# Optimization experiments

Hardware: AMD Instinct MI355X
Metric: run time of the kernel (lower is better)

Reference implementation:

```python
import jax, jax.numpy as jnp
import numpy as np

P_OUT = 2048   # num_output_points
K_NN = 32      # num_neighbors
LEAK = 0.2     # LeakyReLU slope in WeightNet


def setup_inputs() -> dict:
    key = jax.random.key(0)
    k1, k2, k3, k4 = jax.random.split(key, 4)
    B, N, D, Cin, Cout, Cmid = 8, 8192, 3, 128, 256, 16
    return {
        "coordinates": jax.random.uniform(k1, (B, N, D), jnp.float32),
        "features": jax.random.normal(k2, (B, N, Cin), jnp.float32),
        "wn_w": jax.random.normal(k3, (Cmid, D), jnp.float32) * 0.1,
        "wn_b": jnp.zeros((Cmid,), jnp.float32),
        "lin_w": jax.random.normal(k4, (Cout, Cin * Cmid), jnp.float32) * 0.02,
        "lin_b": jnp.zeros((Cout,), jnp.float32),
    }


def _fps(coords, num_out):
    """Deterministic farthest point sampling (initial point = index 0)."""
    B, N, _ = coords.shape

    def step(carry, _):
        dist, far = carry
        centroid = jnp.take_along_axis(coords, far[:, None, None], axis=1)  # (B,1,D)
        d = jnp.linalg.norm(coords - centroid, axis=-1)                     # (B,N)
        dist = jnp.minimum(dist, d)
        return (dist, jnp.argmax(dist, axis=-1)), far

    init = (jnp.full((B, N), 1e10, coords.dtype), jnp.zeros((B,), jnp.int32))
    _, idx = jax.lax.scan(step, init, None, length=num_out)
    return jnp.transpose(idx)  # (B, num_out)


def _knn(k, coords, centers):
    # squared L2 via gram trick; monotone in L2 so top-k indices match torch.cdist+topk
    d2 = (jnp.sum(centers ** 2, -1)[:, :, None]
          + jnp.sum(coords ** 2, -1)[:, None, :]
          - 2.0 * jnp.einsum('bpd,bnd->bpn', centers, coords))
    _, idx = jax.lax.top_k(-d2, k)
    return idx  # (B,P,K)


_gather = jax.vmap(lambda pts, idx: pts[idx])  # index_points equivalent


def reference(coordinates, features, wn_w, wn_b, lin_w, lin_b):
    B = coordinates.shape[0]
    samp_idx = _fps(coordinates, P_OUT)                      # (B,P)
    out_coords = _gather(coordinates, samp_idx)              # (B,P,D)
    nbr_idx = _knn(K_NN, coordinates, out_coords)            # (B,P,K)
    group_coords = _gather(coordinates, nbr_idx)             # (B,P,K,D)
    centered = group_coords - out_coords[:, :, None, :]      # (B,P,K,D)
    group_feat = _gather(features, nbr_idx)                  # (B,P,K,Cin)
    # WeightNet: 1x1-conv MLP (single layer) + LeakyReLU(0.2)
    w = jax.nn.leaky_relu(jnp.einsum('bpkd,md->bpkm', centered, wn_w) + wn_b, LEAK)
    # PointConv aggregation: (B,P,Cin,K) @ (B,P,K,Cmid) -> (B,P,Cin,Cmid) -> flatten
    nf = jnp.einsum('bpkc,bpkm->bpcm', group_feat, w).reshape(B, P_OUT, -1)
    nf = nf @ lin_w.T + lin_b                                # (B,P,Cout)
    return out_coords, nf
```

## Files before the change

### kernel.cpp

```cpp
#include <hip/hip_runtime.h>
#include <hip/hip_bf16.h>

#define NB    8
#define NPTS  8192
#define P_OUT 2048
#define KNN   32
#define CIN   128
#define CMID  16
#define COUT  256

typedef __bf16 bf16x8 __attribute__((ext_vector_type(8)));
typedef float  f32x4  __attribute__((ext_vector_type(4)));
typedef float  f32x2  __attribute__((ext_vector_type(2)));

__device__ __forceinline__ float sqrt_rn_f32(float x) { return (float)sqrt((double)x); }

__device__ __forceinline__ unsigned short f2bf(float x) {
    unsigned u = __float_as_uint(x);
    return (unsigned short)((u + 0x7FFFu + ((u >> 16) & 1u)) >> 16);
}

__device__ __forceinline__ float wave_max_dpp(float x) {
    int v, t;
    v = __float_as_int(x);
    t = __builtin_amdgcn_update_dpp(v, v, 0xB1, 0xF, 0xF, false);
    x = fmaxf(x, __int_as_float(t));
    v = __float_as_int(x);
    t = __builtin_amdgcn_update_dpp(v, v, 0x4E, 0xF, 0xF, false);
    x = fmaxf(x, __int_as_float(t));
    v = __float_as_int(x);
    t = __builtin_amdgcn_update_dpp(v, v, 0x141, 0xF, 0xF, false);
    x = fmaxf(x, __int_as_float(t));
    v = __float_as_int(x);
    t = __builtin_amdgcn_update_dpp(v, v, 0x140, 0xF, 0xF, false);
    x = fmaxf(x, __int_as_float(t));
    v = __float_as_int(x);
    t = __builtin_amdgcn_update_dpp(v, v, 0x142, 0xA, 0xF, false);
    x = fmaxf(x, __int_as_float(t));
    v = __float_as_int(x);
    t = __builtin_amdgcn_update_dpp(v, v, 0x143, 0xC, 0xF, false);
    x = fmaxf(x, __int_as_float(t));
    return x;
}

__global__ __launch_bounds__(256) void prep_kernel(const float* __restrict__ coords,
                                                   const float* __restrict__ lin_w,
                                                   float2* __restrict__ zp,
                                                   unsigned short* __restrict__ lwbf) {
    const int i = blockIdx.x * 256 + threadIdx.x;
    if (i < NB * NPTS) {
        const float* pc = coords + (size_t)i * 3;
        const float x = pc[0], y = pc[1], z = pc[2];
        float t = __fmul_rn(x, x);
        t = __fadd_rn(t, __fmul_rn(y, y));
        t = __fadd_rn(t, __fmul_rn(z, z));
        zp[i] = make_float2(z, t);
    }
    if (i < COUT * CIN * CMID) lwbf[i] = f2bf(lin_w[i]);
}

__global__ __launch_bounds__(512) void fps_kernel(const float* __restrict__ coords,
                                                  float* __restrict__ out_coords) {
    #pragma clang fp contract(off)
    const int b    = blockIdx.x;
    const int tid  = threadIdx.x;
    const int lane = tid & 63;
    const int wv   = tid >> 6;
    const float* cb = coords + (size_t)b * (NPTS * 3);
    float* outc = out_coords + (size_t)b * (P_OUT * 3);

    __shared__ __align__(16) float warr[8];
    __shared__ unsigned winslot;
    __shared__ float csl[3];

    f32x2 pxv[8], pyv[8], pzv[8], d2v[8];
    {
        float buf[48];
        const float4* g4 = (const float4*)cb;
        #pragma unroll
        for (int i = 0; i < 12; ++i) {
            float4 v = g4[tid * 12 + i];
            buf[i*4+0] = v.x; buf[i*4+1] = v.y; buf[i*4+2] = v.z; buf[i*4+3] = v.w;
        }
        #pragma unroll
        for (int i = 0; i < 8; ++i) {
            pxv[i] = f32x2{buf[(2*i)*3+0], buf[(2*i+1)*3+0]};
            pyv[i] = f32x2{buf[(2*i)*3+1], buf[(2*i+1)*3+1]};
            pzv[i] = f32x2{buf[(2*i)*3+2], buf[(2*i+1)*3+2]};
            d2v[i] = f32x2{__builtin_inff(), __builtin_inff()};
        }
    }
    if (tid == 0) {
        csl[0] = pxv[0][0]; csl[1] = pyv[0][0]; csl[2] = pzv[0][0];
        winslot = 0xFFFFFFFFu;
    }
    __syncthreads();
    float cx = csl[0], cy = csl[1], cz = csl[2];
    const unsigned base = (unsigned)tid * 16;

    for (int s = 0; s < P_OUT; ++s) {
        if (tid == 0) { outc[s*3+0] = cx; outc[s*3+1] = cy; outc[s*3+2] = cz; }
        if (s == P_OUT - 1) break;

        const f32x2 cx2 = {cx, cx}, cy2 = {cy, cy}, cz2 = {cz, cz};
        f32x2 tmax2 = {0.0f, 0.0f};
        #pragma unroll
        for (int i = 0; i < 8; ++i) {
            const f32x2 dx = pxv[i] - cx2;
            const f32x2 dy = pyv[i] - cy2;
            const f32x2 dz = pzv[i] - cz2;
            f32x2 t = dx * dx;
            t = t + dy * dy;
            t = t + dz * dz;
            const f32x2 nd = __builtin_elementwise_min(d2v[i], t);
            d2v[i] = nd;
            tmax2 = __builtin_elementwise_max(tmax2, nd);
        }
        const float tmax = fmaxf(tmax2[0], tmax2[1]);

        const float wmaxl = wave_max_dpp(tmax);
        if (lane == 63) warr[wv] = wmaxl;
        __syncthreads();

        const float4 q0 = *(const float4*)(warr + 0);
        const float4 q1 = *(const float4*)(warr + 4);
        const float gmax = fmaxf(fmaxf(fmaxf(q0.x, q0.y), fmaxf(q0.z, q0.w)),
                                 fmaxf(fmaxf(q1.x, q1.y), fmaxf(q1.z, q1.w)));
        const float wmax = (wv < 4) ? ((wv < 2) ? (wv ? q0.y : q0.x) : (wv == 2 ? q0.z : q0.w))
                                    : ((wv < 6) ? (wv == 4 ? q1.x : q1.y) : (wv == 6 ? q1.z : q1.w));

        if (__float_as_uint(wmax) + 3u >= __float_as_uint(gmax)) {
            const float s_ = sqrt_rn_f32(gmax);
            float t_lo = gmax;
            const unsigned gb = __float_as_uint(gmax);
            #pragma unroll
            for (int j = 1; j <= 3; ++j) {
                float v = __uint_as_float(gb - j);
                if (sqrt_rn_f32(v) == s_) t_lo = v;
            }
            unsigned cand = 0xFFFFFFFFu;
            #pragma unroll
            for (int i = 7; i >= 0; --i) {
                if (d2v[i][1] >= t_lo) cand = base + 2*i + 1;
                if (d2v[i][0] >= t_lo) cand = base + 2*i;
            }
            if (cand != 0xFFFFFFFFu) atomicMin(&winslot, cand);
        }
        __syncthreads();

        const unsigned widx = winslot;
        if ((widx >> 4) == (unsigned)tid) {
            #pragma unroll
            for (int i = 0; i < 8; ++i) {
                if (widx == base + 2*i)     { csl[0]=pxv[i][0]; csl[1]=pyv[i][0]; csl[2]=pzv[i][0]; }
                if (widx == base + 2*i + 1) { csl[0]=pxv[i][1]; csl[1]=pyv[i][1]; csl[2]=pzv[i][1]; }
            }
        }
        __syncthreads();
        if (tid == 0) winslot = 0xFFFFFFFFu;
        cx = csl[0]; cy = csl[1]; cz = csl[2];
    }
}

__global__ __launch_bounds__(1024) void knn_kernel(const float* __restrict__ coords,
                                                   const float2* __restrict__ zp,
                                                   const float* __restrict__ out_coords,
                                                   int* __restrict__ nbr) {
    const int b     = blockIdx.x & 7;
    const int chunk = blockIdx.x >> 3;
    const int tid   = threadIdx.x;
    const int wv    = tid >> 6, lane = tid & 63;
    __shared__ float2 sxy[NPTS];
    {
        float buf[24];
        const float4* g4 = (const float4*)(coords + (size_t)b * (NPTS * 3));
        #pragma unroll
        for (int i = 0; i < 6; ++i) {
            float4 v = g4[tid * 6 + i];
            buf[i*4+0]=v.x; buf[i*4+1]=v.y; buf[i*4+2]=v.z; buf[i*4+3]=v.w;
        }
        #pragma unroll
        for (int i = 0; i < 8; ++i)
            sxy[tid*8 + i] = make_float2(buf[i*3+0], buf[i*3+1]);
    }
    __syncthreads();
    const float2* zpb = zp + (size_t)b * NPTS;

    for (int ci = 0; ci < 4; ++ci) {
        const int p = chunk * 64 + wv * 4 + ci;
        const float* oc = out_coords + ((size_t)b * P_OUT + p) * 3;
        const float cx = oc[0], cy = oc[1], cz = oc[2];
        const float cc = __fadd_rn(__fadd_rn(__fmul_rn(cx,cx), __fmul_rn(cy,cy)), __fmul_rn(cz,cz));
        float ld2 = __builtin_inff();
        unsigned lidx = 0x7FFFFFFFu;
        for (int j0 = 0; j0 < NPTS; j0 += 64) {
            const int p2 = j0 + lane;
            const float2 xy = sxy[p2];
            const float2 zq = zpb[p2];
            const float dot = fmaf(cz, zq.x, fmaf(cy, xy.y, __fmul_rn(cx, xy.x)));
            const float d2  = __fsub_rn(__fadd_rn(cc, zq.y), __fmul_rn(2.0f, dot));
            const float    T  = __shfl(ld2, 31, 64);
            const unsigned Ti = __shfl(lidx, 31, 64);
            const bool qf = (d2 < T) || (d2 == T && (unsigned)p2 < Ti);
            unsigned long long mask = __ballot(qf);
            while (mask) {
                const int l = __ffsll(mask) - 1;
                const float    cd2  = __shfl(d2, l, 64);
                const unsigned cidx = (unsigned)(j0 + l);
                float    pv = __shfl_up(ld2, 1, 64);
                unsigned pi = __shfl_up(lidx, 1, 64);
                if (lane == 0) { pv = cd2; pi = cidx; }
                const bool mlt = (ld2 < cd2) || (ld2 == cd2 && lidx < cidx);
                const bool plt = (pv  < cd2) || (pv  == cd2 && pi   < cidx);
                ld2  = mlt ? ld2  : (plt ? cd2  : pv);
                lidx = mlt ? lidx : (plt ? cidx : pi);
                mask &= (mask - 1);
            }
        }
        if (lane < KNN) nbr[((size_t)b * P_OUT + p) * KNN + lane] = (int)lidx;
    }
}

__global__ __launch_bounds__(128) void pconv_kernel(const float* __restrict__ coords,
                                                    const float* __restrict__ feats,
                                                    const float* __restrict__ out_coords,
                                                    const int* __restrict__ nbr,
                                                    const float* __restrict__ wn_w,
                                                    const float* __restrict__ wn_b,
                                                    unsigned short* __restrict__ nf) {
    const int bp  = (blockIdx.x & 7) * P_OUT + (blockIdx.x >> 3);
    const int b   = bp >> 11;
    const int tid = threadIdx.x;
    __shared__ __align__(16) float wmat[32][16];
    __shared__ int nidx[32];
    __shared__ float ctr[3];
    if (tid < 32) nidx[tid] = nbr[(size_t)bp * KNN + tid];
    if (tid < 3)  ctr[tid]  = out_coords[(size_t)bp * 3 + tid];
    __syncthreads();
    {
        const int k  = tid >> 2;
        const int m0 = (tid & 3) * 4;
        const int n  = nidx[k];
        const float* pc = coords + ((size_t)b * NPTS + n) * 3;
        const float dx = pc[0] - ctr[0];
        const float dy = pc[1] - ctr[1];
        const float dz = pc[2] - ctr[2];
        #pragma unroll
        for (int mm = 0; mm < 4; ++mm) {
            const int m = m0 + mm;
            float a = dx * wn_w[m*3+0] + dy * wn_w[m*3+1] + dz * wn_w[m*3+2] + wn_b[m];
            wmat[k][m] = (a >= 0.0f) ? a : 0.2f * a;
        }
    }
    __syncthreads();
    const int c = tid;
    float acc[16];
    #pragma unroll
    for (int m = 0; m < 16; ++m) acc[m] = 0.0f;
    const float* fb = feats + (size_t)b * NPTS * CIN;
    #pragma unroll 4
    for (int k = 0; k < 32; ++k) {
        const float f = fb[(size_t)nidx[k] * CIN + c];
        const float4* wr = (const float4*)(&wmat[k][0]);
        const float4 w0 = wr[0], w1 = wr[1], w2 = wr[2], w3 = wr[3];
        acc[0]  += f * w0.x;  acc[1]  += f * w0.y;  acc[2]  += f * w0.z;  acc[3]  += f * w0.w;
        acc[4]  += f * w1.x;  acc[5]  += f * w1.y;  acc[6]  += f * w1.z;  acc[7]  += f * w1.w;
        acc[8]  += f * w2.x;  acc[9]  += f * w2.y;  acc[10] += f * w2.z;  acc[11] += f * w2.w;
        acc[12] += f * w3.x;  acc[13] += f * w3.y;  acc[14] += f * w3.z;  acc[15] += f * w3.w;
    }
    unsigned u[8];
    #pragma unroll
    for (int m = 0; m < 8; ++m) {
        const unsigned lo = f2bf(acc[2*m]);
        const unsigned hi = f2bf(acc[2*m+1]);
        u[m] = lo | (hi << 16);
    }
    uint4* dst = (uint4*)(nf + (size_t)bp * 2048 + c * 16);
    dst[0] = make_uint4(u[0], u[1], u[2], u[3]);
    dst[1] = make_uint4(u[4], u[5], u[6], u[7]);
}

__global__ __launch_bounds__(256) void gemm_kernel(const unsigned short* __restrict__ A,
                                                   const unsigned short* __restrict__ Bw,
                                                   const float* __restrict__ bias,
                                                   float* __restrict__ C) {
    __shared__ __align__(16) unsigned short Als[128 * 40];
    __shared__ __align__(16) unsigned short Bls[128 * 40];
    const int tid = threadIdx.x;
    const int m0  = blockIdx.x * 128;
    const int cb  = blockIdx.y;
    const int wv  = tid >> 6, lane = tid & 63;
    const int wr  = wv >> 1,  wc   = wv & 1;
    const int sr  = tid >> 1;
    const int ko  = (tid & 1) * 16;
    const int rr  = lane & 15, kg = lane >> 4;

    f32x4 acc[4][4] = {};

    for (int kt = 0; kt < 2048 / 32; ++kt) {
        const uint4* as = (const uint4*)(A  + (size_t)(m0 + sr) * 2048 + kt * 32 + ko);
        const uint4 a0 = as[0], a1 = as[1];
        const uint4* bs = (const uint4*)(Bw + (size_t)(cb * 128 + sr) * 2048 + kt * 32 + ko);
        const uint4 b0 = bs[0], b1 = bs[1];
        __syncthreads();
        *(uint4*)(&Als[sr * 40 + ko])     = a0;
        *(uint4*)(&Als[sr * 40 + ko + 8]) = a1;
        *(uint4*)(&Bls[sr * 40 + ko])     = b0;
        *(uint4*)(&Bls[sr * 40 + ko + 8]) = b1;
        __syncthreads();
        bf16x8 af[4], bfv[4];
        #pragma unroll
        for (int i = 0; i < 4; ++i)
            af[i] = *(const bf16x8*)(&Als[(wr*64 + i*16 + rr) * 40 + kg * 8]);
        #pragma unroll
        for (int j = 0; j < 4; ++j)
            bfv[j] = *(const bf16x8*)(&Bls[(wc*64 + j*16 + rr) * 40 + kg * 8]);
        #pragma unroll
        for (int i = 0; i < 4; ++i)
            #pragma unroll
            for (int j = 0; j < 4; ++j)
                acc[i][j] = __builtin_amdgcn_mfma_f32_16x16x32_bf16(af[i], bfv[j], acc[i][j], 0, 0, 0);
    }
    const int rg = lane >> 4;
    #pragma unroll
    for (int j = 0; j < 4; ++j) {
        const int col = cb * 128 + wc * 64 + j * 16 + rr;
        const float bv = bias[col];
        #pragma unroll
        for (int i = 0; i < 4; ++i) {
            const int row = m0 + wr * 64 + i * 16 + rg * 4;
            #pragma unroll
            for (int g = 0; g < 4; ++g)
                C[(size_t)(row + g) * 256 + col] = acc[i][j][g] + bv;
        }
    }
}

extern "C" void kernel_launch(void* const* d_in, const int* in_sizes, int n_in,
                              void* d_out, int out_size, void* d_ws, size_t ws_size,
                              hipStream_t stream) {
    const float* coords = (const float*)d_in[0];
    const float* feats  = (const float*)d_in[1];
    const float* wn_w   = (const float*)d_in[2];
    const float* wn_b   = (const float*)d_in[3];
    const float* lin_w  = (const float*)d_in[4];
    const float* lin_b  = (const float*)d_in[5];

    float* out        = (float*)d_out;
    float* out_coords = out;
    float* out_nf     = out + NB * P_OUT * 3;

    char* ws = (char*)d_ws;
    int*            nbr  = (int*)ws;
    float2*         zp   = (float2*)(ws + ((size_t)2  << 20));
    unsigned short* lwbf = (unsigned short*)(ws + ((size_t)2560 << 10));
    unsigned short* nf   = (unsigned short*)(ws + ((size_t)4  << 20));

    prep_kernel <<<2048, 256, 0, stream>>>(coords, lin_w, zp, lwbf);
    fps_kernel  <<<NB, 512, 0, stream>>>(coords, out_coords);
    knn_kernel  <<<256, 1024, 0, stream>>>(coords, zp, out_coords, nbr);
    pconv_kernel<<<NB * P_OUT, 128, 0, stream>>>(coords, feats, out_coords, nbr, wn_w, wn_b, nf);
    gemm_kernel <<<dim3(128, 2), 256, 0, stream>>>(nf, lwbf, lin_b, out_nf);
}
```

Before: 3.528 ms.

## Cut FPS per-step barriers via double-buffered winner slot and global centroid reload

The FPS loop now double-buffers the atomic winner slot so that resetting it no longer needs its own barrier. The new centroid is read straight from global coordinates by every thread, which replaces the shared-memory broadcast and the third __syncthreads per step. The sqrt-based threshold is computed from the wave-local max before the barrier, hiding that latency. In exchange, each step adds a dependent global (likely L1/L2-hit) load on the serial critical path.

```diff
diff --git a/kernel.cpp b/kernel.cpp
--- a/kernel.cpp
+++ b/kernel.cpp
@@ -70,8 +70,7 @@
     float* outc = out_coords + (size_t)b * (P_OUT * 3);
 
     __shared__ __align__(16) float warr[8];
-    __shared__ unsigned winslot;
-    __shared__ float csl[3];
+    __shared__ unsigned winslot[2];
 
     f32x2 pxv[8], pyv[8], pzv[8], d2v[8];
     {
@@ -90,12 +89,9 @@
             d2v[i] = f32x2{__builtin_inff(), __builtin_inff()};
         }
     }
-    if (tid == 0) {
-        csl[0] = pxv[0][0]; csl[1] = pyv[0][0]; csl[2] = pzv[0][0];
-        winslot = 0xFFFFFFFFu;
-    }
+    if (tid == 0) { winslot[0] = 0xFFFFFFFFu; winslot[1] = 0xFFFFFFFFu; }
+    float cx = cb[0], cy = cb[1], cz = cb[2];
     __syncthreads();
-    float cx = csl[0], cy = csl[1], cz = csl[2];
     const unsigned base = (unsigned)tid * 16;
 
     for (int s = 0; s < P_OUT; ++s) {
@@ -120,23 +116,37 @@
 
         const float wmaxl = wave_max_dpp(tmax);
         if (lane == 63) warr[wv] = wmaxl;
+        const float wmax = __shfl(wmaxl, 63, 64);
+
+        const unsigned wb = __float_as_uint(wmax);
+        const float s_sp = sqrt_rn_f32(wmax);
+        float t_lo_sp = wmax;
+        #pragma unroll
+        for (int j = 1; j <= 3; ++j) {
+            const float v = __uint_as_float(wb - j);
+            if (sqrt_rn_f32(v) == s_sp) t_lo_sp = v;
+        }
         __syncthreads();
+        if (tid == 0) winslot[(s + 1) & 1] = 0xFFFFFFFFu;
 
         const float4 q0 = *(const float4*)(warr + 0);
         const float4 q1 = *(const float4*)(warr + 4);
         const float gmax = fmaxf(fmaxf(fmaxf(q0.x, q0.y), fmaxf(q0.z, q0.w)),
                                  fmaxf(fmaxf(q1.x, q1.y), fmaxf(q1.z, q1.w)));
-        const float wmax = (wv < 4) ? ((wv < 2) ? (wv ? q0.y : q0.x) : (wv == 2 ? q0.z : q0.w))
-                                    : ((wv < 6) ? (wv == 4 ? q1.x : q1.y) : (wv == 6 ? q1.z : q1.w));
-
-        if (__float_as_uint(wmax) + 3u >= __float_as_uint(gmax)) {
-            const float s_ = sqrt_rn_f32(gmax);
-            float t_lo = gmax;
-            const unsigned gb = __float_as_uint(gmax);
-            #pragma unroll
-            for (int j = 1; j <= 3; ++j) {
-                float v = __uint_as_float(gb - j);
-                if (sqrt_rn_f32(v) == s_) t_lo = v;
+
+        if (wb + 3u >= __float_as_uint(gmax)) {
+            float t_lo;
+            if (wmax == gmax) {
+                t_lo = t_lo_sp;
+            } else {
+                const float s_ = sqrt_rn_f32(gmax);
+                const unsigned gb = __float_as_uint(gmax);
+                t_lo = gmax;
+                #pragma unroll
+                for (int j = 1; j <= 3; ++j) {
+                    const float v = __uint_as_float(gb - j);
+                    if (sqrt_rn_f32(v) == s_) t_lo = v;
+                }
             }
             unsigned cand = 0xFFFFFFFFu;
             #pragma unroll
@@ -144,21 +154,14 @@
                 if (d2v[i][1] >= t_lo) cand = base + 2*i + 1;
                 if (d2v[i][0] >= t_lo) cand = base + 2*i;
             }
-            if (cand != 0xFFFFFFFFu) atomicMin(&winslot, cand);
+            if (cand != 0xFFFFFFFFu) atomicMin(&winslot[s & 1], cand);
         }
         __syncthreads();
 
-        const unsigned widx = winslot;
-        if ((widx >> 4) == (unsigned)tid) {
-            #pragma unroll
-            for (int i = 0; i < 8; ++i) {
-                if (widx == base + 2*i)     { csl[0]=pxv[i][0]; csl[1]=pyv[i][0]; csl[2]=pzv[i][0]; }
-                if (widx == base + 2*i + 1) { csl[0]=pxv[i][1]; csl[1]=pyv[i][1]; csl[2]=pzv[i][1]; }
-            }
-        }
-        __syncthreads();
-        if (tid == 0) winslot = 0xFFFFFFFFu;
-        cx = csl[0]; cy = csl[1]; cz = csl[2];
+        const unsigned widx = winslot[s & 1];
+        cx = cb[widx * 3 + 0];
+        cy = cb[widx * 3 + 1];
+        cz = cb[widx * 3 + 2];
     }
 }
 
```

Result: faster. 3.048 ms (-13.6%).
